# Kernel tuning notes

Hardware: AMD Instinct MI355X
Metric: run time of the kernel (lower is better)

Reference implementation:

```python
import jax, jax.numpy as jnp
import numpy as np

SCALE = 64.0
MARGIN = 0.5
EPS_CLAMP = 1e-7
EPS_NORM = 1e-12

N, D, C = 4096, 512, 30000


def setup_inputs() -> dict:
    key = jax.random.key(0)
    k1, k2, k3 = jax.random.split(key, 3)
    embeddings = jax.random.normal(k1, (N, D), dtype=jnp.float32)
    classifier_weights = jax.random.normal(k2, (C, D), dtype=jnp.float32)
    labels = jax.random.randint(k3, (N,), 0, C, dtype=jnp.int64)
    return {"embeddings": embeddings, "labels": labels, "classifier_weights": classifier_weights}


def reference(embeddings, labels, classifier_weights):
    # F.normalize(classifier_weights): L2-normalize each class row (dim=1)
    norm = jnp.linalg.norm(classifier_weights, axis=1, keepdims=True)
    w_norm = classifier_weights / jnp.maximum(norm, EPS_NORM)
    # cosine similarity logits: [N, C]  (embeddings are NOT normalized in source)
    cosine = jnp.einsum("nd,cd->nc", embeddings, w_norm)
    # angle with margin added only at the target class
    angle = jnp.arccos(jnp.clip(cosine, -1.0 + EPS_CLAMP, 1.0 - EPS_CLAMP))
    one_hot = jax.nn.one_hot(labels, C, dtype=cosine.dtype)
    logits = jnp.cos(angle + MARGIN * one_hot) * SCALE
    # mean cross-entropy
    logp = jax.nn.log_softmax(logits, axis=-1)
    nll = -jnp.take_along_axis(logp, labels[:, None], axis=1)[:, 0]
    return jnp.mean(nll)
```

## Files before the change

kernel.cpp:

```cpp
#include <hip/hip_runtime.h>
#include <cstdint>
#include <cstddef>

#define N_ROWS 4096
#define DIM    512
#define NCLS   30000
#define BM 256
#define BN 256
#define BK 32
#define NT2  118
#define CPAD (NT2 * 256)
#define SPT 2
#define NSTRIPS (NT2 / SPT)
#define KT  (DIM / BK)
#define NS  (SPT * KT)

typedef float  f32x4  __attribute__((ext_vector_type(4)));
typedef short  bf16x8 __attribute__((ext_vector_type(8)));
typedef unsigned int   u32;
typedef unsigned short u16;

#define WB_BYTES   ((size_t)CPAD * DIM * 2)
#define EB_BYTES   ((size_t)N_ROWS * DIM * 2)
#define PS_BYTES   ((size_t)NT2 * N_ROWS * 4)
#define CT_BYTES   ((size_t)N_ROWS * 4)
#define BL_BYTES   (64 * 4)
#define LAB_BYTES  ((size_t)N_ROWS * 4)

#define CLIP_HI ( 1.0f - 1e-7f)
#define CLIP_LO (-1.0f + 1e-7f)
#define COSM 0.8775825618903728f
#define SINM 0.4794255386042030f
#define K1   92.33248261972189f

__device__ __forceinline__ u16 f2bf(float f) {
  u32 x = __builtin_bit_cast(u32, f);
  x += 0x7fffu + ((x >> 16) & 1u);
  return (u16)(x >> 16);
}

__device__ __forceinline__ void gl_lds16(const u16* g, u16* l) {
  __builtin_amdgcn_global_load_lds((const __attribute__((address_space(1))) u32*)g,
                                   (__attribute__((address_space(3))) u32*)l,
                                   16, 0, 0);
}

__global__ void lab_detect(const int* __restrict__ lab, int* __restrict__ flag) {
  __shared__ int s_nz;
  int tid = threadIdx.x;
  if (tid == 0) s_nz = 0;
  __syncthreads();
  int nz = 0;
  for (int i = tid; i < N_ROWS / 2; i += 1024) nz |= lab[2 * i + 1];
  if (nz) atomicOr(&s_nz, 1);
  __syncthreads();
  if (tid == 0) *flag = (s_nz == 0) ? 1 : 0;
}

__global__ void lab_fix(const int* __restrict__ lab, const int* __restrict__ flag,
                        int* __restrict__ out) {
  int i = blockIdx.x * 256 + threadIdx.x;
  out[i] = flag[0] ? lab[2 * i] : lab[i];
}

__global__ void prep_w(const float* __restrict__ w, u16* __restrict__ wb) {
  int wv   = threadIdx.x >> 6;
  int lane = threadIdx.x & 63;
  int c = blockIdx.x * 4 + wv;
  u16* dst = wb + (size_t)c * DIM + lane * 8;
  if (c >= NCLS) {
    *(uint4*)dst = make_uint4(0, 0, 0, 0);
    return;
  }
  const float* src = w + (size_t)c * DIM + lane * 8;
  float4 v0 = *(const float4*)src;
  float4 v1 = *(const float4*)(src + 4);
  float a[8] = {v0.x, v0.y, v0.z, v0.w, v1.x, v1.y, v1.z, v1.w};
  float ss = 0.f;
  #pragma unroll
  for (int i = 0; i < 8; i++) ss += a[i] * a[i];
  #pragma unroll
  for (int off = 32; off; off >>= 1) ss += __shfl_xor(ss, off, 64);
  float inv = 1.0f / fmaxf(sqrtf(ss), 1e-12f);
  union { u16 h[8]; uint4 q; } pk;
  #pragma unroll
  for (int i = 0; i < 8; i++) pk.h[i] = f2bf(a[i] * inv);
  *(uint4*)dst = pk.q;
}

__global__ void prep_e(const float* __restrict__ e, u16* __restrict__ eb) {
  size_t idx = ((size_t)blockIdx.x * 256 + threadIdx.x) * 8;
  float4 v0 = *(const float4*)(e + idx);
  float4 v1 = *(const float4*)(e + idx + 4);
  float a[8] = {v0.x, v0.y, v0.z, v0.w, v1.x, v1.y, v1.z, v1.w};
  union { u16 h[8]; uint4 q; } pk;
  #pragma unroll
  for (int i = 0; i < 8; i++) pk.h[i] = f2bf(a[i]);
  *(uint4*)(eb + idx) = pk.q;
}

__global__ void tgt_k(const float* __restrict__ emb, const float* __restrict__ wts,
                      const int* __restrict__ lab, float* __restrict__ ct) {
  int w = threadIdx.x >> 6, l = threadIdx.x & 63;
  int row = blockIdx.x * 4 + w;
  int c = lab[row];
  const float* e  = emb + (size_t)row * DIM + l * 8;
  const float* wp = wts + (size_t)c   * DIM + l * 8;
  float4 e0 = *(const float4*)e,       e1 = *(const float4*)(e + 4);
  float4 w0 = *(const float4*)wp,      w1 = *(const float4*)(wp + 4);
  float dot = e0.x*w0.x + e0.y*w0.y + e0.z*w0.z + e0.w*w0.w
            + e1.x*w1.x + e1.y*w1.y + e1.z*w1.z + e1.w*w1.w;
  float ss  = w0.x*w0.x + w0.y*w0.y + w0.z*w0.z + w0.w*w0.w
            + w1.x*w1.x + w1.y*w1.y + w1.z*w1.z + w1.w*w1.w;
  #pragma unroll
  for (int off = 32; off; off >>= 1) {
    dot += __shfl_xor(dot, off, 64);
    ss  += __shfl_xor(ss,  off, 64);
  }
  if (l == 0) ct[row] = dot / fmaxf(sqrtf(ss), 1e-12f);
}

__global__ __launch_bounds__(512, 2) void arc_main(
    const u16* __restrict__ eb, const u16* __restrict__ wb,
    float* __restrict__ psum)
{
  __shared__ __align__(16) u16 lA[3][BM * BK];
  __shared__ __align__(16) u16 lB[3][BN * BK];
  __shared__ float ep[4][BM];
  const int tid = threadIdx.x;
  const int l   = tid & 63;
  const int w   = tid >> 6;
  const int wm  = w >> 2, wn = w & 3;
  const int mi    = blockIdx.x & 15;
  const int strip = blockIdx.x >> 4;
  const int rowbase = mi * BM;
  const int n0 = strip * SPT;

  u32 aoff[8], boff[4];
  const int bq = l >> 4;
  #pragma unroll
  for (int m = 0; m < 8; m++) {
    int r = wm * 128 + m * 16 + (l & 15);
    aoff[m] = (u32)r * BK + ((bq ^ ((r >> 1) & 3)) << 3);
  }
  #pragma unroll
  for (int n = 0; n < 4; n++) {
    int r = wn * 64 + n * 16 + (l & 15);
    boff[n] = (u32)r * BK + ((bq ^ ((r >> 1) & 3)) << 3);
  }

  const int sch = (w & 3) * 4;
  u32 goff[4];
  #pragma unroll
  for (int i = 0; i < 4; i++) {
    int rl = (sch + i) * 16 + (l >> 2);
    goff[i] = (u32)rl * DIM + (((l & 3) ^ ((rl >> 1) & 3)) << 3);
  }
  const bool isA = (w < 4);
  const u16* gsrc = isA ? (eb + (size_t)rowbase * DIM) : wb;
  u16* lds0 = isA ? &lA[0][0] : &lB[0][0];

  #define STAGE(u_) do {                                                     \
    const int buf_ = (u_) % 3;                                               \
    const u32 base_ = isA ? (u32)(((u_) & 15) * BK)                          \
        : (u32)(n0 + ((u_) >> 4)) * BN * DIM + (u32)(((u_) & 15) * BK);      \
    u16* dst_ = lds0 + buf_ * (BM * BK) + sch * 512;                         \
    _Pragma("unroll")                                                        \
    for (int i_ = 0; i_ < 4; i_++)                                           \
      gl_lds16(gsrc + base_ + goff[i_], dst_ + i_ * 512);                    \
  } while (0)

  f32x4 acc[8][4];
  #pragma unroll
  for (int m = 0; m < 8; m++)
    #pragma unroll
    for (int n = 0; n < 4; n++)
      #pragma unroll
      for (int q = 0; q < 4; q++) acc[m][n][q] = 0.f;

  STAGE(0);
  STAGE(1);

  for (int u = 0; u < NS; u++) {
    if (u < NS - 1) asm volatile("s_waitcnt vmcnt(4)" ::: "memory");
    else            asm volatile("s_waitcnt vmcnt(0)" ::: "memory");
    __builtin_amdgcn_s_barrier();
    asm volatile("" ::: "memory");
    if (u + 2 < NS) STAGE(u + 2);

    const int buf = u % 3;
    bf16x8 af[8], bg[4];
    #pragma unroll
    for (int m = 0; m < 8; m++) af[m] = *(const bf16x8*)&lA[buf][aoff[m]];
    #pragma unroll
    for (int n = 0; n < 4; n++) bg[n] = *(const bf16x8*)&lB[buf][boff[n]];

    __builtin_amdgcn_s_setprio(1);
    #pragma unroll
    for (int m = 0; m < 8; m++)
      #pragma unroll
      for (int n = 0; n < 4; n++)
        acc[m][n] = __builtin_amdgcn_mfma_f32_16x16x32_bf16(af[m], bg[n], acc[m][n], 0, 0, 0);
    __builtin_amdgcn_s_setprio(0);

    if ((u & 15) == 15) {
      const int nt = n0 + (u >> 4);
      #pragma unroll
      for (int m = 0; m < 8; m++) {
        #pragma unroll
        for (int q = 0; q < 4; q++) {
          float s = 0.f;
          #pragma unroll
          for (int n = 0; n < 4; n++) {
            float tc = __builtin_amdgcn_fmed3f(acc[m][n][q], CLIP_LO, CLIP_HI);
            s += __builtin_amdgcn_exp2f(__builtin_fmaf(tc, K1, -K1));
            acc[m][n][q] = 0.f;
          }
          s += __shfl_xor(s, 1, 64);
          s += __shfl_xor(s, 2, 64);
          s += __shfl_xor(s, 4, 64);
          s += __shfl_xor(s, 8, 64);
          if ((l & 15) == 0) ep[wn][wm * 128 + m * 16 + (l >> 4) * 4 + q] = s;
        }
      }
      asm volatile("s_waitcnt lgkmcnt(0)" ::: "memory");
      __builtin_amdgcn_s_barrier();
      asm volatile("" ::: "memory");
      if (l < 32) {
        int r = w * 32 + l;
        float t = ep[0][r] + ep[1][r] + ep[2][r] + ep[3][r];
        psum[(size_t)nt * N_ROWS + rowbase + r] = t;
      }
    }
  }
  #undef STAGE
}

__global__ void arc_finish1(const float* __restrict__ psum, const float* __restrict__ ct,
                            float* __restrict__ bl) {
  int tid = threadIdx.x;
  int row = blockIdx.x * 256 + tid;
  float S = 0.f;
  for (int p = 0; p < NT2; p++) S += psum[(size_t)p * N_ROWS + row];
  float c  = __builtin_amdgcn_fmed3f(ct[row], CLIP_LO, CLIP_HI);
  float cm = c * COSM - sqrtf(fmaxf(1.0f - c * c, 0.0f)) * SINM;
  float S2 = S - __builtin_amdgcn_exp2f(__builtin_fmaf(c,  K1, -K1))
               + __builtin_amdgcn_exp2f(__builtin_fmaf(cm, K1, -K1));
  float loss = 64.0f + __builtin_amdgcn_logf(S2) * 0.6931471805599453f - 64.0f * cm;
  #pragma unroll
  for (int off = 32; off; off >>= 1) loss += __shfl_xor(loss, off, 64);
  __shared__ float red[4];
  if ((tid & 63) == 0) red[tid >> 6] = loss;
  __syncthreads();
  if (tid == 0) bl[blockIdx.x] = red[0] + red[1] + red[2] + red[3];
}

__global__ void arc_finish2(const float* __restrict__ bl, float* __restrict__ out) {
  if (threadIdx.x == 0) {
    float t = 0.f;
    for (int i = 0; i < N_ROWS / 256; i++) t += bl[i];
    out[0] = t * (1.0f / (float)N_ROWS);
  }
}

extern "C" void kernel_launch(void* const* d_in, const int* in_sizes, int n_in,
                              void* d_out, int out_size, void* d_ws, size_t ws_size,
                              hipStream_t stream) {
  const float* emb   = (const float*)d_in[0];
  const int*   lab   = (const int*)d_in[1];
  const float* wts   = (const float*)d_in[2];

  char* ws = (char*)d_ws;
  u16*   wb    = (u16*)(ws);
  u16*   eb    = (u16*)(ws + WB_BYTES);
  float* psum  = (float*)(ws + WB_BYTES + EB_BYTES);
  float* ct    = (float*)(ws + WB_BYTES + EB_BYTES + PS_BYTES);
  float* bl    = (float*)(ws + WB_BYTES + EB_BYTES + PS_BYTES + CT_BYTES);
  int*   lab32 = (int*)  (ws + WB_BYTES + EB_BYTES + PS_BYTES + CT_BYTES + BL_BYTES);
  int*   flag  = (int*)  (ws + WB_BYTES + EB_BYTES + PS_BYTES + CT_BYTES + BL_BYTES + LAB_BYTES);

  lab_detect<<<dim3(1), dim3(1024), 0, stream>>>(lab, flag);
  lab_fix<<<dim3(N_ROWS / 256), dim3(256), 0, stream>>>(lab, flag, lab32);
  prep_w<<<dim3(CPAD / 4), dim3(256), 0, stream>>>(wts, wb);
  prep_e<<<dim3((N_ROWS * DIM / 8) / 256), dim3(256), 0, stream>>>(emb, eb);
  tgt_k<<<dim3(N_ROWS / 4), dim3(256), 0, stream>>>(emb, wts, lab32, ct);
  arc_main<<<dim3(16 * NSTRIPS), dim3(512), 0, stream>>>(eb, wb, psum);
  arc_finish1<<<dim3(N_ROWS / 256), dim3(256), 0, stream>>>(psum, ct, bl);
  arc_finish2<<<dim3(1), dim3(64), 0, stream>>>(bl, (float*)d_out);
}
```

Before: 214.8 us.

## Double-buffer LDS and register fragments to overlap LDS reads with MFMA

Replaces the three-stage LDS ring, where A and B loads were split between wave groups, with a two-buffer LDS layout in which every thread loads both A and B tiles. MFMA fragments are now double-buffered in registers, so the next k-step's fragments are read from LDS while the current step's MFMAs run. The goal is to hide LDS read latency behind the matrix units. In exchange it doubles the fragment registers, which risks spills or lower occupancy at the current launch bounds. It also adds a full-block sync after each epilogue and waits for vmcnt(0) every step, leaving less global prefetch depth.

```diff
diff --git a/kernel.cpp b/kernel.cpp
--- a/kernel.cpp
+++ b/kernel.cpp
@@ -12,8 +12,7 @@
 #define CPAD (NT2 * 256)
 #define SPT 2
 #define NSTRIPS (NT2 / SPT)
-#define KT  (DIM / BK)
-#define NS  (SPT * KT)
+#define NS  (SPT * (DIM / BK))
 
 typedef float  f32x4  __attribute__((ext_vector_type(4)));
 typedef short  bf16x8 __attribute__((ext_vector_type(8)));
@@ -124,51 +123,27 @@
     const u16* __restrict__ eb, const u16* __restrict__ wb,
     float* __restrict__ psum)
 {
-  __shared__ __align__(16) u16 lA[3][BM * BK];
-  __shared__ __align__(16) u16 lB[3][BN * BK];
+  __shared__ __align__(16) u16 lds[32768];
   __shared__ float ep[4][BM];
-  const int tid = threadIdx.x;
-  const int l   = tid & 63;
-  const int w   = tid >> 6;
-  const int wm  = w >> 2, wn = w & 3;
+  const int t  = threadIdx.x;
+  const int l  = t & 63;
+  const int w  = t >> 6;
+  const int wm = w >> 2, wn = w & 3;
+  const int cl = l & 15, bq = l >> 4;
   const int mi    = blockIdx.x & 15;
   const int strip = blockIdx.x >> 4;
   const int rowbase = mi * BM;
-  const int n0 = strip * SPT;
-
-  u32 aoff[8], boff[4];
-  const int bq = l >> 4;
-  #pragma unroll
-  for (int m = 0; m < 8; m++) {
-    int r = wm * 128 + m * 16 + (l & 15);
-    aoff[m] = (u32)r * BK + ((bq ^ ((r >> 1) & 3)) << 3);
-  }
-  #pragma unroll
-  for (int n = 0; n < 4; n++) {
-    int r = wn * 64 + n * 16 + (l & 15);
-    boff[n] = (u32)r * BK + ((bq ^ ((r >> 1) & 3)) << 3);
-  }
-
-  const int sch = (w & 3) * 4;
-  u32 goff[4];
-  #pragma unroll
-  for (int i = 0; i < 4; i++) {
-    int rl = (sch + i) * 16 + (l >> 2);
-    goff[i] = (u32)rl * DIM + (((l & 3) ^ ((rl >> 1) & 3)) << 3);
-  }
-  const bool isA = (w < 4);
-  const u16* gsrc = isA ? (eb + (size_t)rowbase * DIM) : wb;
-  u16* lds0 = isA ? &lA[0][0] : &lB[0][0];
-
-  #define STAGE(u_) do {                                                     \
-    const int buf_ = (u_) % 3;                                               \
-    const u32 base_ = isA ? (u32)(((u_) & 15) * BK)                          \
-        : (u32)(n0 + ((u_) >> 4)) * BN * DIM + (u32)(((u_) & 15) * BK);      \
-    u16* dst_ = lds0 + buf_ * (BM * BK) + sch * 512;                         \
-    _Pragma("unroll")                                                        \
-    for (int i_ = 0; i_ < 4; i_++)                                           \
-      gl_lds16(gsrc + base_ + goff[i_], dst_ + i_ * 512);                    \
-  } while (0)
+  const int n0s = strip * SPT;
+
+  const u32 so    = (u32)((bq ^ ((cl >> 1) & 3)) << 3);
+  const u32 aBase = (u32)(wm * 128 + cl) * 32 + so;
+  const u32 bBase = (u32)(wn * 64  + cl) * 32 + so;
+
+  const u32 ssl = (u32)(((t & 3) ^ ((t >> 3) & 3)) << 3);
+  const u32 g0  = (u32)(t >> 2) * DIM + ssl;
+  const u32 g1  = (u32)(128 + (t >> 2)) * DIM + ssl;
+  const u32 t8  = (u32)t * 8;
+  const u16* ebR = eb + (size_t)rowbase * DIM;
 
   f32x4 acc[8][4];
   #pragma unroll
@@ -178,33 +153,66 @@
       #pragma unroll
       for (int q = 0; q < 4; q++) acc[m][n][q] = 0.f;
 
-  STAGE(0);
-  STAGE(1);
-
-  for (int u = 0; u < NS; u++) {
-    if (u < NS - 1) asm volatile("s_waitcnt vmcnt(4)" ::: "memory");
-    else            asm volatile("s_waitcnt vmcnt(0)" ::: "memory");
-    __builtin_amdgcn_s_barrier();
-    asm volatile("" ::: "memory");
-    if (u + 2 < NS) STAGE(u + 2);
-
-    const int buf = u % 3;
-    bf16x8 af[8], bg[4];
-    #pragma unroll
-    for (int m = 0; m < 8; m++) af[m] = *(const bf16x8*)&lA[buf][aoff[m]];
-    #pragma unroll
-    for (int n = 0; n < 4; n++) bg[n] = *(const bf16x8*)&lB[buf][boff[n]];
-
-    __builtin_amdgcn_s_setprio(1);
-    #pragma unroll
-    for (int m = 0; m < 8; m++)
-      #pragma unroll
-      for (int n = 0; n < 4; n++)
-        acc[m][n] = __builtin_amdgcn_mfma_f32_16x16x32_bf16(af[m], bg[n], acc[m][n], 0, 0, 0);
-    __builtin_amdgcn_s_setprio(0);
-
-    if ((u & 15) == 15) {
-      const int nt = n0 + (u >> 4);
+  {
+    const u32 b0 = (u32)n0s * (BN * DIM);
+    gl_lds16(ebR + g0,            &lds[t8]);
+    gl_lds16(ebR + g1,            &lds[4096 + t8]);
+    gl_lds16(wb + b0 + g0,        &lds[16384 + t8]);
+    gl_lds16(wb + b0 + g1,        &lds[16384 + 4096 + t8]);
+    gl_lds16(ebR + 32 + g0,       &lds[8192 + t8]);
+    gl_lds16(ebR + 32 + g1,       &lds[8192 + 4096 + t8]);
+    gl_lds16(wb + b0 + 32 + g0,   &lds[24576 + t8]);
+    gl_lds16(wb + b0 + 32 + g1,   &lds[24576 + 4096 + t8]);
+  }
+  asm volatile("s_waitcnt vmcnt(4)" ::: "memory");
+  __builtin_amdgcn_s_barrier();
+  asm volatile("" ::: "memory");
+
+  bf16x8 fA0[8], fB0[4], fA1[8], fB1[4];
+  #pragma unroll
+  for (int m = 0; m < 8; m++) fA0[m] = *(const bf16x8*)&lds[aBase + m * 512];
+  #pragma unroll
+  for (int n = 0; n < 4; n++) fB0[n] = *(const bf16x8*)&lds[16384 + bBase + n * 512];
+
+  #define STEP(u_, PAR, FAr, FBr, FAw, FBw) do {                              \
+    asm volatile("s_waitcnt vmcnt(0)" ::: "memory");                          \
+    __builtin_amdgcn_s_barrier();                                             \
+    asm volatile("" ::: "memory");                                            \
+    if ((u_) + 2 < NS) {                                                      \
+      const u32 k2_ = (u32)(((u_) + 2) & 15) * 32;                            \
+      const u32 b2_ = (u32)(n0s + (((u_) + 2) >> 4)) * (BN * DIM) + k2_;      \
+      gl_lds16(ebR + k2_ + g0, &lds[(PAR) * 8192 + t8]);                      \
+      gl_lds16(ebR + k2_ + g1, &lds[(PAR) * 8192 + 4096 + t8]);               \
+      gl_lds16(wb + b2_ + g0,  &lds[16384 + (PAR) * 8192 + t8]);              \
+      gl_lds16(wb + b2_ + g1,  &lds[16384 + (PAR) * 8192 + 4096 + t8]);       \
+    }                                                                         \
+    {                                                                         \
+      const u16* Ar_ = &lds[(1 - (PAR)) * 8192];                              \
+      const u16* Br_ = &lds[16384 + (1 - (PAR)) * 8192];                      \
+      _Pragma("unroll")                                                       \
+      for (int m_ = 0; m_ < 8; m_++)                                          \
+        FAw[m_] = *(const bf16x8*)&Ar_[aBase + m_ * 512];                     \
+      _Pragma("unroll")                                                       \
+      for (int n_ = 0; n_ < 4; n_++)                                          \
+        FBw[n_] = *(const bf16x8*)&Br_[bBase + n_ * 512];                     \
+    }                                                                         \
+    __builtin_amdgcn_s_setprio(1);                                            \
+    _Pragma("unroll")                                                         \
+    for (int m_ = 0; m_ < 8; m_++)                                            \
+      _Pragma("unroll")                                                       \
+      for (int n_ = 0; n_ < 4; n_++)                                          \
+        acc[m_][n_] = __builtin_amdgcn_mfma_f32_16x16x32_bf16(                \
+            FAr[m_], FBr[n_], acc[m_][n_], 0, 0, 0);                          \
+    __builtin_amdgcn_s_setprio(0);                                            \
+  } while (0)
+
+  for (int p = 0; p < NS / 2; p++) {
+    const int u0 = 2 * p;
+    STEP(u0,     0, fA0, fB0, fA1, fB1);
+    STEP(u0 + 1, 1, fA1, fB1, fA0, fB0);
+
+    if ((p & 7) == 7) {
+      const int nt = n0s + (p >> 3);
       #pragma unroll
       for (int m = 0; m < 8; m++) {
         #pragma unroll
@@ -223,17 +231,16 @@
           if ((l & 15) == 0) ep[wn][wm * 128 + m * 16 + (l >> 4) * 4 + q] = s;
         }
       }
-      asm volatile("s_waitcnt lgkmcnt(0)" ::: "memory");
-      __builtin_amdgcn_s_barrier();
-      asm volatile("" ::: "memory");
+      __syncthreads();
       if (l < 32) {
         int r = w * 32 + l;
-        float t = ep[0][r] + ep[1][r] + ep[2][r] + ep[3][r];
-        psum[(size_t)nt * N_ROWS + rowbase + r] = t;
+        float v = ep[0][r] + ep[1][r] + ep[2][r] + ep[3][r];
+        psum[(size_t)nt * N_ROWS + rowbase + r] = v;
       }
+      __syncthreads();
     }
   }
-  #undef STAGE
+  #undef STEP
 }
 
 __global__ void arc_finish1(const float* __restrict__ psum, const float* __restrict__ ct,
```

Result: no change. 214.9 us (+0.1%).

## Restructure GEMM pipeline to 4-slot LDS ring with unrolled compile-time buffer indexing

Applied to the files above, without the earlier changes.

Replaces the triple-buffered lA/lB arrays with one raw shared buffer holding a 4-slot ring, unrolls the K loop by four so buffer offsets are compile-time constants, and has all waves load both A and B tiles instead of splitting them by wave. The goal is to remove modulo-3 address math and per-fragment offset registers. LDS use grows to about 132 KB and the occupancy hint of 2 is dropped, so likely one workgroup per CU. An extra barrier after the epilogue protects reuse of the ep scratch region.

```diff
diff --git a/kernel.cpp b/kernel.cpp
--- a/kernel.cpp
+++ b/kernel.cpp
@@ -12,8 +12,7 @@
 #define CPAD (NT2 * 256)
 #define SPT 2
 #define NSTRIPS (NT2 / SPT)
-#define KT  (DIM / BK)
-#define NS  (SPT * KT)
+#define NS  (SPT * (DIM / BK))
 
 typedef float  f32x4  __attribute__((ext_vector_type(4)));
 typedef short  bf16x8 __attribute__((ext_vector_type(8)));
@@ -120,55 +119,31 @@
   if (l == 0) ct[row] = dot / fmaxf(sqrtf(ss), 1e-12f);
 }
 
-__global__ __launch_bounds__(512, 2) void arc_main(
+__global__ __launch_bounds__(512) void arc_main(
     const u16* __restrict__ eb, const u16* __restrict__ wb,
     float* __restrict__ psum)
 {
-  __shared__ __align__(16) u16 lA[3][BM * BK];
-  __shared__ __align__(16) u16 lB[3][BN * BK];
-  __shared__ float ep[4][BM];
-  const int tid = threadIdx.x;
-  const int l   = tid & 63;
-  const int w   = tid >> 6;
-  const int wm  = w >> 2, wn = w & 3;
+  __shared__ __align__(16) char smem[135168];
+  const int t  = threadIdx.x;
+  const int l  = t & 63;
+  const int w  = t >> 6;
+  const int wm = w >> 2, wn = w & 3;
+  const int cl = l & 15, bq = l >> 4;
   const int mi    = blockIdx.x & 15;
   const int strip = blockIdx.x >> 4;
   const int rowbase = mi * BM;
-  const int n0 = strip * SPT;
-
-  u32 aoff[8], boff[4];
-  const int bq = l >> 4;
-  #pragma unroll
-  for (int m = 0; m < 8; m++) {
-    int r = wm * 128 + m * 16 + (l & 15);
-    aoff[m] = (u32)r * BK + ((bq ^ ((r >> 1) & 3)) << 3);
-  }
-  #pragma unroll
-  for (int n = 0; n < 4; n++) {
-    int r = wn * 64 + n * 16 + (l & 15);
-    boff[n] = (u32)r * BK + ((bq ^ ((r >> 1) & 3)) << 3);
-  }
-
-  const int sch = (w & 3) * 4;
-  u32 goff[4];
-  #pragma unroll
-  for (int i = 0; i < 4; i++) {
-    int rl = (sch + i) * 16 + (l >> 2);
-    goff[i] = (u32)rl * DIM + (((l & 3) ^ ((rl >> 1) & 3)) << 3);
-  }
-  const bool isA = (w < 4);
-  const u16* gsrc = isA ? (eb + (size_t)rowbase * DIM) : wb;
-  u16* lds0 = isA ? &lA[0][0] : &lB[0][0];
-
-  #define STAGE(u_) do {                                                     \
-    const int buf_ = (u_) % 3;                                               \
-    const u32 base_ = isA ? (u32)(((u_) & 15) * BK)                          \
-        : (u32)(n0 + ((u_) >> 4)) * BN * DIM + (u32)(((u_) & 15) * BK);      \
-    u16* dst_ = lds0 + buf_ * (BM * BK) + sch * 512;                         \
-    _Pragma("unroll")                                                        \
-    for (int i_ = 0; i_ < 4; i_++)                                           \
-      gl_lds16(gsrc + base_ + goff[i_], dst_ + i_ * 512);                    \
-  } while (0)
+  const int n0s = strip * SPT;
+
+  const u32 swz = (u32)((bq ^ ((cl >> 1) & 3)) << 3);
+  const u32 aB  = ((u32)(wm * 128 + cl) * 32 + swz) * 2;
+  const u32 bB  = 65536u + ((u32)(wn * 64 + cl) * 32 + swz) * 2;
+
+  const u32 ssl = (u32)(((t & 3) ^ ((t >> 3) & 3)) << 3);
+  const u32 g0  = (u32)(t >> 2) * DIM + ssl;
+  const u32 g1  = (u32)(128 + (t >> 2)) * DIM + ssl;
+  const u32 tb  = (u32)t * 16;
+  const u16* ebR = eb + (size_t)rowbase * DIM;
+  const u16* wbS = wb + (size_t)n0s * (BN * DIM);
 
   f32x4 acc[8][4];
   #pragma unroll
@@ -178,62 +153,90 @@
       #pragma unroll
       for (int q = 0; q < 4; q++) acc[m][n][q] = 0.f;
 
-  STAGE(0);
-  STAGE(1);
-
-  for (int u = 0; u < NS; u++) {
-    if (u < NS - 1) asm volatile("s_waitcnt vmcnt(4)" ::: "memory");
-    else            asm volatile("s_waitcnt vmcnt(0)" ::: "memory");
-    __builtin_amdgcn_s_barrier();
-    asm volatile("" ::: "memory");
-    if (u + 2 < NS) STAGE(u + 2);
-
-    const int buf = u % 3;
-    bf16x8 af[8], bg[4];
+  #pragma unroll
+  for (int v = 0; v < 2; v++) {
+    gl_lds16(ebR + v * 32 + g0, (u16*)(smem + v * 16384 + tb));
+    gl_lds16(ebR + v * 32 + g1, (u16*)(smem + v * 16384 + 8192 + tb));
+    gl_lds16(wbS + v * 32 + g0, (u16*)(smem + 65536 + v * 16384 + tb));
+    gl_lds16(wbS + v * 32 + g1, (u16*)(smem + 65536 + v * 16384 + 8192 + tb));
+  }
+  asm volatile("s_waitcnt vmcnt(4)" ::: "memory");
+  __builtin_amdgcn_s_barrier();
+  asm volatile("" ::: "memory");
+
+  for (int u0 = 0; u0 < NS; u0 += 4) {
     #pragma unroll
-    for (int m = 0; m < 8; m++) af[m] = *(const bf16x8*)&lA[buf][aoff[m]];
-    #pragma unroll
-    for (int n = 0; n < 4; n++) bg[n] = *(const bf16x8*)&lB[buf][boff[n]];
-
-    __builtin_amdgcn_s_setprio(1);
-    #pragma unroll
-    for (int m = 0; m < 8; m++)
-      #pragma unroll
-      for (int n = 0; n < 4; n++)
-        acc[m][n] = __builtin_amdgcn_mfma_f32_16x16x32_bf16(af[m], bg[n], acc[m][n], 0, 0, 0);
-    __builtin_amdgcn_s_setprio(0);
-
-    if ((u & 15) == 15) {
-      const int nt = n0 + (u >> 4);
-      #pragma unroll
-      for (int m = 0; m < 8; m++) {
-        #pragma unroll
-        for (int q = 0; q < 4; q++) {
-          float s = 0.f;
-          #pragma unroll
-          for (int n = 0; n < 4; n++) {
-            float tc = __builtin_amdgcn_fmed3f(acc[m][n][q], CLIP_LO, CLIP_HI);
-            s += __builtin_amdgcn_exp2f(__builtin_fmaf(tc, K1, -K1));
-            acc[m][n][q] = 0.f;
-          }
-          s += __shfl_xor(s, 1, 64);
-          s += __shfl_xor(s, 2, 64);
-          s += __shfl_xor(s, 4, 64);
-          s += __shfl_xor(s, 8, 64);
-          if ((l & 15) == 0) ep[wn][wm * 128 + m * 16 + (l >> 4) * 4 + q] = s;
-        }
-      }
-      asm volatile("s_waitcnt lgkmcnt(0)" ::: "memory");
+    for (int j = 0; j < 4; j++) {
+      const int u = u0 + j;
+
+      if (u < NS - 1) asm volatile("s_waitcnt vmcnt(4)" ::: "memory");
+      else            asm volatile("s_waitcnt vmcnt(0)" ::: "memory");
       __builtin_amdgcn_s_barrier();
       asm volatile("" ::: "memory");
-      if (l < 32) {
-        int r = w * 32 + l;
-        float t = ep[0][r] + ep[1][r] + ep[2][r] + ep[3][r];
-        psum[(size_t)nt * N_ROWS + rowbase + r] = t;
+
+      if (u + 2 < NS) {
+        const int v = u + 2;
+        const u32 ka = (u32)(v & 15) * 32;
+        const u16* bsrc = wbS + (size_t)(v >> 4) * (BN * DIM) + ka;
+        char* dA = smem + ((j + 2) & 3) * 16384;
+        char* dB = smem + 65536 + ((j + 2) & 3) * 16384;
+        gl_lds16(ebR + ka + g0, (u16*)(dA + tb));
+        gl_lds16(ebR + ka + g1, (u16*)(dA + 8192 + tb));
+        gl_lds16(bsrc + g0,     (u16*)(dB + tb));
+        gl_lds16(bsrc + g1,     (u16*)(dB + 8192 + tb));
+      }
+
+      bf16x8 af[8], bg[4];
+      #pragma unroll
+      for (int m = 0; m < 8; m++)
+        af[m] = *(const bf16x8*)(smem + j * 16384 + aB + m * 1024);
+      #pragma unroll
+      for (int n = 0; n < 4; n++)
+        bg[n] = *(const bf16x8*)(smem + j * 16384 + bB + n * 1024);
+
+      __builtin_amdgcn_s_setprio(1);
+      #pragma unroll
+      for (int m = 0; m < 8; m++)
+        #pragma unroll
+        for (int n = 0; n < 4; n++)
+          acc[m][n] = __builtin_amdgcn_mfma_f32_16x16x32_bf16(af[m], bg[n], acc[m][n], 0, 0, 0);
+      __builtin_amdgcn_s_setprio(0);
+
+      if (j == 3 && (u0 & 15) == 12) {
+        const int nt = n0s + (u >> 4);
+        float* ep = (float*)(smem + 131072);
+        #pragma unroll
+        for (int m = 0; m < 8; m++) {
+          #pragma unroll
+          for (int q = 0; q < 4; q++) {
+            float s = 0.f;
+            #pragma unroll
+            for (int n = 0; n < 4; n++) {
+              float tc = __builtin_amdgcn_fmed3f(acc[m][n][q], CLIP_LO, CLIP_HI);
+              s += __builtin_amdgcn_exp2f(__builtin_fmaf(tc, K1, -K1));
+              acc[m][n][q] = 0.f;
+            }
+            s += __shfl_xor(s, 1, 64);
+            s += __shfl_xor(s, 2, 64);
+            s += __shfl_xor(s, 4, 64);
+            s += __shfl_xor(s, 8, 64);
+            if ((l & 15) == 0) ep[wn * 256 + wm * 128 + m * 16 + (l >> 4) * 4 + q] = s;
+          }
+        }
+        asm volatile("s_waitcnt lgkmcnt(0)" ::: "memory");
+        __builtin_amdgcn_s_barrier();
+        asm volatile("" ::: "memory");
+        if (l < 32) {
+          int r = w * 32 + l;
+          float v = ep[r] + ep[256 + r] + ep[512 + r] + ep[768 + r];
+          psum[(size_t)nt * N_ROWS + rowbase + r] = v;
+        }
+        asm volatile("" ::: "memory");
+        __builtin_amdgcn_s_barrier();
+        asm volatile("" ::: "memory");
       }
     }
   }
-  #undef STAGE
 }
 
 __global__ void arc_finish1(const float* __restrict__ psum, const float* __restrict__ ct,
```

New measurement: 213.1 us. No clear change (-0.8%).
